# Optimization experiments

Hardware: AMD Instinct MI355X
Metric: run time of the kernel (lower is better)

The kernel has to match this reference:

```python
import jax, jax.numpy as jnp
import numpy as np
import math

FEATURE_DIM = 512
CLASS_NUM = 100000
BATCH = 512
SCALE = 30.0
MARGIN = 0.5
# easy_margin=False branch: Threshholder=-cos(margin), out_indicator=1
THRESHOLD = -math.cos(MARGIN)
OUT_INDICATOR = 1.0


def setup_inputs() -> dict:
    key = jax.random.key(0)
    k_feat, k_w, k_lab = jax.random.split(key, 3)
    feat = jax.random.normal(k_feat, (BATCH, FEATURE_DIM), dtype=jnp.float32)
    # xavier_uniform init for weights [class_num, feature_dim]
    limit = math.sqrt(6.0 / (CLASS_NUM + FEATURE_DIM))
    weights = jax.random.uniform(k_w, (CLASS_NUM, FEATURE_DIM), dtype=jnp.float32,
                                 minval=-limit, maxval=limit)
    label = jax.random.randint(k_lab, (BATCH,), 0, CLASS_NUM, dtype=jnp.int64)
    return {"feat": feat, "weights": weights, "label": label}


def reference(feat, weights, label):
    # Normalize features and weights
    norm_feat = jnp.linalg.norm(feat, axis=-1, keepdims=True)          # [B,1]
    nfeat = feat / norm_feat                                           # [B,D]
    norm_w = jnp.linalg.norm(weights, axis=-1, keepdims=True)          # [C,1]
    nw = weights / norm_w                                              # [C,D]

    cos = jnp.matmul(nfeat, nw.T)                                      # [B,C]

    avg_w_norm = jnp.mean(norm_w)
    avg_x_norm = jnp.mean(norm_feat)

    b = feat.shape[0]
    rows = jnp.arange(b)
    cos_label = cos[rows, label]                                       # [B]

    # per-sample angle stats (degrees), vectorized replacement of the python loop
    thetas = jnp.arccos(cos_label) / jnp.pi * 180.0
    avg_theta = jnp.mean(thetas)
    min_theta = jnp.min(thetas)
    max_theta = jnp.max(thetas)
    stdv_theta = jnp.sqrt(jnp.sum((thetas - avg_theta) ** 2) / (b - 1))

    # margin tables: add margin at label column if cos > threshold, else additive penalty
    in_margin = cos_label > THRESHOLD                                  # [B] bool
    margin_vals = jnp.where(in_margin, MARGIN, 0.0).astype(cos.dtype)
    ext_vals = jnp.where(in_margin, 0.0, -MARGIN * math.sin(MARGIN)).astype(cos.dtype)
    margin_tables = jnp.zeros_like(cos).at[rows, label].set(margin_vals)
    margin_tables_ext = (jnp.zeros_like(cos).at[rows, label].set(ext_vals)) * OUT_INDICATOR

    marginal_logits = SCALE * (jnp.cos(jnp.arccos(cos) + margin_tables) + margin_tables_ext)

    return (cos, marginal_logits, avg_theta, min_theta, max_theta,
            stdv_theta, avg_w_norm, avg_x_norm)
```

## Files before the change

kernel.cpp:

```cpp
#include <hip/hip_runtime.h>
#include <hip/hip_bf16.h>

#define FEATURE_DIM 512
#define CLASS_NUM   100000
#define BATCH       512
#define NTILE       128
#define NBLK        782
#define SCALE       30.0f
#define MARGIN      0.5f

typedef unsigned short u16;
typedef __attribute__((ext_vector_type(8))) short bf16x8;
typedef __attribute__((ext_vector_type(4))) float f32x4;

__device__ __forceinline__ u16 f32_to_bf16(float f) {
    unsigned int x = __builtin_bit_cast(unsigned int, f);
    unsigned int r = (x + 0x7fffu + ((x >> 16) & 1u)) >> 16;
    return (u16)r;
}

#define GLL(g, l) __builtin_amdgcn_global_load_lds( \
    (const __attribute__((address_space(1))) void*)(g), \
    (__attribute__((address_space(3))) void*)(l), 16, 0, 0)

__global__ __launch_bounds__(256) void normalize_rows(
    const float* __restrict__ src, u16* __restrict__ dst,
    float* __restrict__ partials, int R)
{
    const int tid  = threadIdx.x;
    const int wid  = tid >> 6;
    const int lane = tid & 63;
    const int row  = blockIdx.x * 4 + wid;
    __shared__ float s_norm[4];

    float norm = 0.0f;
    u16* drow = dst + (size_t)row * FEATURE_DIM;
    if (row < R) {
        const float4* p = (const float4*)(src + (size_t)row * FEATURE_DIM);
        float4 a = p[lane];
        float4 b = p[lane + 64];
        float ss = a.x*a.x + a.y*a.y + a.z*a.z + a.w*a.w
                 + b.x*b.x + b.y*b.y + b.z*b.z + b.w*b.w;
        #pragma unroll
        for (int o = 32; o > 0; o >>= 1) ss += __shfl_xor(ss, o, 64);
        norm = sqrtf(ss);
        float inv = 1.0f / norm;
        ushort4 pa, pb;
        pa.x = f32_to_bf16(a.x * inv); pa.y = f32_to_bf16(a.y * inv);
        pa.z = f32_to_bf16(a.z * inv); pa.w = f32_to_bf16(a.w * inv);
        pb.x = f32_to_bf16(b.x * inv); pb.y = f32_to_bf16(b.y * inv);
        pb.z = f32_to_bf16(b.z * inv); pb.w = f32_to_bf16(b.w * inv);
        ushort4* q = (ushort4*)drow;
        q[lane]      = pa;
        q[lane + 64] = pb;
    }
    if (lane == 0) s_norm[wid] = norm;
    __syncthreads();
    if (tid == 0)
        partials[blockIdx.x] = s_norm[0] + s_norm[1] + s_norm[2] + s_norm[3];
}

__global__ __launch_bounds__(512, 2) void gemm_fused(
    const u16*  __restrict__ A,
    const float* __restrict__ W,
    float* __restrict__ cosO, float* __restrict__ logO,
    float* __restrict__ pw)
{
    __shared__ u16 As[512 * 32];
    __shared__ u16 Bs[128 * 32];
    __shared__ float s_inv[128];
    __shared__ float s_red[8];

    const int tid  = threadIdx.x;
    const int n0   = blockIdx.x * NTILE;
    const int wid  = tid >> 6;
    const int lane = tid & 63;
    const int wm   = (wid & 3) << 7;
    const int wn   = (wid >> 2) << 6;
    const int quad = lane >> 4;
    const int l15  = lane & 15;

    f32x4 acc[8][4];
    #pragma unroll
    for (int i = 0; i < 8; ++i)
        #pragma unroll
        for (int j = 0; j < 4; ++j)
            acc[i][j] = (f32x4){0.f, 0.f, 0.f, 0.f};

    const int srow = tid >> 2;
    const int scol = (tid & 3) * 8;
    const u16* gA = A + (size_t)srow * FEATURE_DIM + scol;
    u16* lA = As + (size_t)tid * 8;

    const int   brow = n0 + srow;
    const bool  bval = brow < CLASS_NUM;
    const float* gW  = W + (size_t)brow * FEATURE_DIM + scol;

    float ssq = 0.0f;

    for (int k0 = 0; k0 < FEATURE_DIM; k0 += 32) {
        GLL(gA + k0,                       lA);
        GLL(gA + k0 + 128 * FEATURE_DIM,  lA + 4096);
        GLL(gA + k0 + 256 * FEATURE_DIM,  lA + 8192);
        GLL(gA + k0 + 384 * FEATURE_DIM,  lA + 12288);

        float4 b0 = {0.f, 0.f, 0.f, 0.f};
        float4 b1 = {0.f, 0.f, 0.f, 0.f};
        if (bval) {
            const float4* p = (const float4*)(gW + k0);
            b0 = p[0];
            b1 = p[1];
        }
        ssq += b0.x*b0.x + b0.y*b0.y + b0.z*b0.z + b0.w*b0.w
             + b1.x*b1.x + b1.y*b1.y + b1.z*b1.z + b1.w*b1.w;
        bf16x8 bb;
        bb[0] = (short)f32_to_bf16(b0.x); bb[1] = (short)f32_to_bf16(b0.y);
        bb[2] = (short)f32_to_bf16(b0.z); bb[3] = (short)f32_to_bf16(b0.w);
        bb[4] = (short)f32_to_bf16(b1.x); bb[5] = (short)f32_to_bf16(b1.y);
        bb[6] = (short)f32_to_bf16(b1.z); bb[7] = (short)f32_to_bf16(b1.w);
        *(bf16x8*)(Bs + (size_t)tid * 8) = bb;

        __syncthreads();

        bf16x8 af[8], bfr[4];
        #pragma unroll
        for (int mi = 0; mi < 8; ++mi)
            af[mi] = *(const bf16x8*)(As + (wm + mi * 16 + l15) * 32 + quad * 8);
        #pragma unroll
        for (int ni = 0; ni < 4; ++ni)
            bfr[ni] = *(const bf16x8*)(Bs + (wn + ni * 16 + l15) * 32 + quad * 8);

        #pragma unroll
        for (int mi = 0; mi < 8; ++mi)
            #pragma unroll
            for (int ni = 0; ni < 4; ++ni)
                acc[mi][ni] = __builtin_amdgcn_mfma_f32_16x16x32_bf16(
                    af[mi], bfr[ni], acc[mi][ni], 0, 0, 0);

        __syncthreads();
    }

    ssq += __shfl_xor(ssq, 1, 64);
    ssq += __shfl_xor(ssq, 2, 64);
    float norm = bval ? sqrtf(ssq) : 0.0f;
    if ((tid & 3) == 0)
        s_inv[srow] = bval ? (1.0f / norm) : 0.0f;

    float nv = ((tid & 3) == 0) ? norm : 0.0f;
    #pragma unroll
    for (int o = 32; o > 0; o >>= 1) nv += __shfl_xor(nv, o, 64);
    if (lane == 0) s_red[wid] = nv;
    __syncthreads();
    if (tid == 0) {
        float t = 0.f;
        #pragma unroll
        for (int i = 0; i < 8; ++i) t += s_red[i];
        pw[blockIdx.x] = t;
    }

    #pragma unroll
    for (int ni = 0; ni < 4; ++ni) {
        int c  = wn + ni * 16 + l15;
        int gc = n0 + c;
        if (gc < CLASS_NUM) {
            float invc = s_inv[c];
            #pragma unroll
            for (int mi = 0; mi < 8; ++mi) {
                int gr0 = wm + mi * 16 + quad * 4;
                f32x4 v = acc[mi][ni];
                #pragma unroll
                for (int r = 0; r < 4; ++r) {
                    float cv = v[r] * invc;
                    size_t idx = (size_t)(gr0 + r) * CLASS_NUM + gc;
                    cosO[idx] = cv;
                    logO[idx] = SCALE * cv;
                }
            }
        }
    }
}

__global__ __launch_bounds__(512) void stats_kernel(
    const float* __restrict__ cosO, float* __restrict__ logO,
    const int* __restrict__ label,
    const float* __restrict__ pw, int npw,
    const float* __restrict__ px, int npx,
    float* __restrict__ scal)
{
    const int tid  = threadIdx.x;
    const int wid  = tid >> 6;
    const int lane = tid & 63;

    __shared__ float r_sum[8], r_min[8], r_max[8], r_w[8], r_x[8], r_var[8];
    __shared__ float s_avg;

    int lab = label[tid];
    lab = max(0, min(CLASS_NUM - 1, lab));
    float x = cosO[(size_t)tid * CLASS_NUM + lab];

    const float cosm = 0.8775825618903728f;
    const float sinm = 0.4794255386042030f;
    float lg;
    if (x > -cosm)
        lg = SCALE * (x * cosm - sinm * sqrtf(fmaxf(0.f, 1.f - x * x)));
    else
        lg = SCALE * (x - MARGIN * sinm);
    logO[(size_t)tid * CLASS_NUM + lab] = lg;

    float xc = fminf(1.f, fmaxf(-1.f, x));
    float theta = acosf(xc) * 57.29577951308232f;

    float sw = 0.f;
    for (int i = tid; i < npw; i += 512) sw += pw[i];
    float sx = (tid < npx) ? px[tid] : 0.f;

    float s = theta, mn = theta, mx = theta;
    #pragma unroll
    for (int o = 32; o > 0; o >>= 1) {
        s  += __shfl_xor(s, o, 64);
        mn  = fminf(mn, __shfl_xor(mn, o, 64));
        mx  = fmaxf(mx, __shfl_xor(mx, o, 64));
        sw += __shfl_xor(sw, o, 64);
        sx += __shfl_xor(sx, o, 64);
    }
    if (lane == 0) {
        r_sum[wid] = s; r_min[wid] = mn; r_max[wid] = mx;
        r_w[wid] = sw; r_x[wid] = sx;
    }
    __syncthreads();
    if (tid == 0) {
        float ts = 0.f, tmn = r_min[0], tmx = r_max[0], tw = 0.f, tx = 0.f;
        #pragma unroll
        for (int i = 0; i < 8; ++i) {
            ts += r_sum[i];
            tmn = fminf(tmn, r_min[i]);
            tmx = fmaxf(tmx, r_max[i]);
            tw += r_w[i];
            tx += r_x[i];
        }
        float avg = ts * (1.0f / BATCH);
        s_avg = avg;
        scal[0] = avg;
        scal[1] = tmn;
        scal[2] = tmx;
        scal[4] = tw * (1.0f / CLASS_NUM);
        scal[5] = tx * (1.0f / BATCH);
    }
    __syncthreads();
    float d = theta - s_avg;
    float v = d * d;
    #pragma unroll
    for (int o = 32; o > 0; o >>= 1) v += __shfl_xor(v, o, 64);
    if (lane == 0) r_var[wid] = v;
    __syncthreads();
    if (tid == 0) {
        float tv = 0.f;
        #pragma unroll
        for (int i = 0; i < 8; ++i) tv += r_var[i];
        scal[3] = sqrtf(tv / (BATCH - 1));
    }
}

extern "C" void kernel_launch(void* const* d_in, const int* in_sizes, int n_in,
                              void* d_out, int out_size, void* d_ws, size_t ws_size,
                              hipStream_t stream)
{
    const float* feat    = (const float*)d_in[0];
    const float* weights = (const float*)d_in[1];
    const int*   label   = (const int*)d_in[2];

    float* out  = (float*)d_out;
    float* cosO = out;
    float* logO = out + (size_t)BATCH * CLASS_NUM;
    float* scal = out + 2 * (size_t)BATCH * CLASS_NUM;

    const size_t nfeat_bytes = (size_t)BATCH * FEATURE_DIM * sizeof(u16);
    const size_t need = nfeat_bytes + (128 + NBLK) * sizeof(float);
    if (ws_size < need) return;

    char*  ws    = (char*)d_ws;
    u16*   nfeat = (u16*)ws;
    float* px    = (float*)(ws + nfeat_bytes);
    float* pw    = px + 128;

    normalize_rows<<<BATCH / 4, 256, 0, stream>>>(feat, nfeat, px, BATCH);

    gemm_fused<<<NBLK, 512, 0, stream>>>(nfeat, weights, cosO, logO, pw);

    stats_kernel<<<1, 512, 0, stream>>>(cosO, logO, label,
                                        pw, NBLK, px, BATCH / 4, scal);
}
```

Baseline: 673.7 us.

## Split GEMM along batch into two M-halves to double grid and cut registers

Each GEMM block now computes a 256-row half of the batch instead of all 512 rows, with a 2D grid (2 x NBLK). This halves the accumulator registers and A-tile LDS per block, which could raise occupancy and the number of blocks available to fill the CUs. In exchange, every weight tile is read from global memory, converted and squared-summed twice, and only the x==0 blocks write the weight norm partials.

```diff
diff --git a/kernel.cpp b/kernel.cpp
--- a/kernel.cpp
+++ b/kernel.cpp
@@ -66,31 +66,33 @@
     float* __restrict__ cosO, float* __restrict__ logO,
     float* __restrict__ pw)
 {
-    __shared__ u16 As[512 * 32];
+    __shared__ u16 As[256 * 32];
     __shared__ u16 Bs[128 * 32];
     __shared__ float s_inv[128];
     __shared__ float s_red[8];
 
     const int tid  = threadIdx.x;
-    const int n0   = blockIdx.x * NTILE;
+    const int m0   = blockIdx.x * 256;
+    const int n0   = blockIdx.y * NTILE;
     const int wid  = tid >> 6;
     const int lane = tid & 63;
-    const int wm   = (wid & 3) << 7;
+    const int wm   = (wid & 3) << 6;
     const int wn   = (wid >> 2) << 6;
     const int quad = lane >> 4;
     const int l15  = lane & 15;
 
-    f32x4 acc[8][4];
-    #pragma unroll
-    for (int i = 0; i < 8; ++i)
+    f32x4 acc[4][4];
+    #pragma unroll
+    for (int i = 0; i < 4; ++i)
         #pragma unroll
         for (int j = 0; j < 4; ++j)
             acc[i][j] = (f32x4){0.f, 0.f, 0.f, 0.f};
 
     const int srow = tid >> 2;
     const int scol = (tid & 3) * 8;
-    const u16* gA = A + (size_t)srow * FEATURE_DIM + scol;
-    u16* lA = As + (size_t)tid * 8;
+    const u16* gA0 = A + (size_t)(m0 + srow) * FEATURE_DIM + scol;
+    u16* lA0 = As + (size_t)tid * 8;
+    u16* lA1 = As + (size_t)(512 + tid) * 8;
 
     const int   brow = n0 + srow;
     const bool  bval = brow < CLASS_NUM;
@@ -99,10 +101,8 @@
     float ssq = 0.0f;
 
     for (int k0 = 0; k0 < FEATURE_DIM; k0 += 32) {
-        GLL(gA + k0,                       lA);
-        GLL(gA + k0 + 128 * FEATURE_DIM,  lA + 4096);
-        GLL(gA + k0 + 256 * FEATURE_DIM,  lA + 8192);
-        GLL(gA + k0 + 384 * FEATURE_DIM,  lA + 12288);
+        GLL(gA0 + k0,                      lA0);
+        GLL(gA0 + k0 + 128 * FEATURE_DIM, lA1);
 
         float4 b0 = {0.f, 0.f, 0.f, 0.f};
         float4 b1 = {0.f, 0.f, 0.f, 0.f};
@@ -122,20 +122,19 @@
 
         __syncthreads();
 
-        bf16x8 af[8], bfr[4];
-        #pragma unroll
-        for (int mi = 0; mi < 8; ++mi)
-            af[mi] = *(const bf16x8*)(As + (wm + mi * 16 + l15) * 32 + quad * 8);
+        bf16x8 bfr[4];
         #pragma unroll
         for (int ni = 0; ni < 4; ++ni)
             bfr[ni] = *(const bf16x8*)(Bs + (wn + ni * 16 + l15) * 32 + quad * 8);
 
         #pragma unroll
-        for (int mi = 0; mi < 8; ++mi)
+        for (int mi = 0; mi < 4; ++mi) {
+            bf16x8 af = *(const bf16x8*)(As + (wm + mi * 16 + l15) * 32 + quad * 8);
             #pragma unroll
             for (int ni = 0; ni < 4; ++ni)
                 acc[mi][ni] = __builtin_amdgcn_mfma_f32_16x16x32_bf16(
-                    af[mi], bfr[ni], acc[mi][ni], 0, 0, 0);
+                    af, bfr[ni], acc[mi][ni], 0, 0, 0);
+        }
 
         __syncthreads();
     }
@@ -146,16 +145,18 @@
     if ((tid & 3) == 0)
         s_inv[srow] = bval ? (1.0f / norm) : 0.0f;
 
-    float nv = ((tid & 3) == 0) ? norm : 0.0f;
-    #pragma unroll
-    for (int o = 32; o > 0; o >>= 1) nv += __shfl_xor(nv, o, 64);
-    if (lane == 0) s_red[wid] = nv;
-    __syncthreads();
-    if (tid == 0) {
+    if (blockIdx.x == 0) {
+        float nv = ((tid & 3) == 0) ? norm : 0.0f;
+        #pragma unroll
+        for (int o = 32; o > 0; o >>= 1) nv += __shfl_xor(nv, o, 64);
+        if (lane == 0) s_red[wid] = nv;
+    }
+    __syncthreads();
+    if (blockIdx.x == 0 && tid == 0) {
         float t = 0.f;
         #pragma unroll
         for (int i = 0; i < 8; ++i) t += s_red[i];
-        pw[blockIdx.x] = t;
+        pw[blockIdx.y] = t;
     }
 
     #pragma unroll
@@ -165,8 +166,8 @@
         if (gc < CLASS_NUM) {
             float invc = s_inv[c];
             #pragma unroll
-            for (int mi = 0; mi < 8; ++mi) {
-                int gr0 = wm + mi * 16 + quad * 4;
+            for (int mi = 0; mi < 4; ++mi) {
+                int gr0 = m0 + wm + mi * 16 + quad * 4;
                 f32x4 v = acc[mi][ni];
                 #pragma unroll
                 for (int r = 0; r < 4; ++r) {
@@ -285,7 +286,8 @@
 
     normalize_rows<<<BATCH / 4, 256, 0, stream>>>(feat, nfeat, px, BATCH);
 
-    gemm_fused<<<NBLK, 512, 0, stream>>>(nfeat, weights, cosO, logO, pw);
+    dim3 grid(2, NBLK);
+    gemm_fused<<<grid, 512, 0, stream>>>(nfeat, weights, cosO, logO, pw);
 
     stats_kernel<<<1, 512, 0, stream>>>(cosO, logO, label,
                                         pw, NBLK, px, BATCH / 4, scal);
```

Measured after the change: 644.9 us. 1.04x faster.
